# Performance work log

Hardware: AMD Instinct MI355X
Metric: run time of the kernel (lower is better)

The kernel has to match this reference:

```python
import jax, jax.numpy as jnp
import numpy as np

B, S, H = 2, 2048, 2048
NH = 16
HD = H // NH          # 128
ROT = HD // 4         # rotary_dim = head_dim * 0.25 = 32
VP = 320              # v_proj_dim
BASE = 10000.0


def setup_inputs() -> dict:
    key = jax.random.key(0)
    ks = jax.random.split(key, 10)
    sc = lambda fan_in: 1.0 / np.sqrt(fan_in)
    return {
        "hidden_states": jax.random.normal(ks[0], (B, S, H), jnp.float32),
        "Wqkv": jax.random.normal(ks[1], (3 * H, H), jnp.float32) * sc(H),
        "bqkv": jnp.zeros((3 * H,), jnp.float32),
        "Wc": jax.random.normal(ks[2], (VP, H), jnp.float32) * sc(H),
        "bc": jnp.zeros((VP,), jnp.float32),
        "Wr": jax.random.normal(ks[3], (H, VP), jnp.float32) * sc(VP),
        "br": jnp.zeros((H,), jnp.float32),
        "Wd": jax.random.normal(ks[4], (H, H), jnp.float32) * sc(H),
        "bd": jnp.zeros((H,), jnp.float32),
    }


def _rope_tables(seq_len, rot_dim, dtype):
    inv_freq = 1.0 / (BASE ** (jnp.arange(0, rot_dim, 2, dtype=jnp.float32) / rot_dim))
    t = jnp.arange(seq_len, dtype=jnp.float32)
    freqs = jnp.outer(t, inv_freq)                      # [S, rot/2]
    emb = jnp.concatenate([freqs, freqs], axis=-1)      # [S, rot]
    return jnp.cos(emb).astype(dtype), jnp.sin(emb).astype(dtype)


def _rotate_half(x):
    x1, x2 = jnp.split(x, 2, axis=-1)
    return jnp.concatenate([-x2, x1], axis=-1)


def reference(hidden_states, Wqkv, bqkv, Wc, bc, Wr, br, Wd, bd):
    b, s, h = hidden_states.shape
    qkv = hidden_states @ Wqkv.T + bqkv                 # [B,S,3H]
    qkv = qkv.reshape(b, s, 3, NH, HD)
    qkv = jnp.transpose(qkv, (2, 0, 3, 1, 4))           # [3,B,NH,S,HD]
    q, k, v = qkv[0], qkv[1], qkv[2]

    cos, sin = _rope_tables(s, ROT, hidden_states.dtype)  # [S,ROT]
    cos = cos[None, None, :, :]
    sin = sin[None, None, :, :]
    q_rot, q_pass = q[..., :ROT], q[..., ROT:]
    k_rot, k_pass = k[..., :ROT], k[..., ROT:]
    q_rot = q_rot * cos + _rotate_half(q_rot) * sin
    k_rot = k_rot * cos + _rotate_half(k_rot) * sin
    q = jnp.concatenate([q_rot, q_pass], axis=-1)
    k = jnp.concatenate([k_rot, k_pass], axis=-1)

    # V low-rank compress / restore
    v_hidden = jnp.transpose(v, (0, 2, 1, 3)).reshape(b, s, h)  # [B,S,H]
    v_restored = (v_hidden @ Wc.T + bc) @ Wr.T + br             # [B,S,H]
    v_heads = jnp.transpose(v_restored.reshape(b, s, NH, HD), (0, 2, 1, 3))  # [B,NH,S,HD]

    scale = HD ** -0.5
    scores = jnp.einsum('bhqd,bhkd->bhqk', q, k) * scale
    causal = jnp.triu(jnp.full((s, s), -jnp.inf, scores.dtype), k=1)
    scores = scores + causal
    attn = jax.nn.softmax(scores, axis=-1)
    out = jnp.einsum('bhqk,bhkd->bhqd', attn, v_heads)
    out = jnp.transpose(out, (0, 2, 1, 3)).reshape(b, s, h)
    return out @ Wd.T + bd
```

## Files before the change

kernel.cpp:

```cpp
#include <hip/hip_runtime.h>

typedef unsigned short u16;
typedef unsigned int u32;
typedef __bf16 bf16x8 __attribute__((ext_vector_type(8)));
typedef float f32x4 __attribute__((ext_vector_type(4)));

#define BB 2
#define SS 2048
#define HH 2048
#define NHH 16
#define HDD 128

__device__ __forceinline__ float b2f(u16 u) {
  union { u32 i; float f; } v; v.i = ((u32)u) << 16; return v.f;
}
__device__ __forceinline__ u16 f2b(float f) {
  union { float f; u32 i; } v; v.f = f;
  u32 x = v.i;
  u32 r = (x + 0x7fffu + ((x >> 16) & 1u)) >> 16;
  return (u16)r;
}

__device__ __forceinline__ void gload_lds16(const u16* g, u16* l) {
  __builtin_amdgcn_global_load_lds(
      (const __attribute__((address_space(1))) u32*)g,
      (__attribute__((address_space(3))) u32*)l, 16, 0, 0);
}

__global__ __launch_bounds__(256) void cvt_kernel(
    const float* __restrict__ s0, u16* __restrict__ d0, int n0,
    const float* __restrict__ s1, u16* __restrict__ d1, int n1,
    const float* __restrict__ s2, u16* __restrict__ d2, int n2,
    const float* __restrict__ s3, u16* __restrict__ d3, int n3,
    const float* __restrict__ s4, u16* __restrict__ d4, int n4)
{
  const float* s; u16* d; int n;
  switch (blockIdx.y) {
    case 0: s = s0; d = d0; n = n0; break;
    case 1: s = s1; d = d1; n = n1; break;
    case 2: s = s2; d = d2; n = n2; break;
    case 3: s = s3; d = d3; n = n3; break;
    default: s = s4; d = d4; n = n4; break;
  }
  int nq = n >> 2;
  for (int q = blockIdx.x * 256 + threadIdx.x; q < nq; q += gridDim.x * 256) {
    float4 v = *(const float4*)(s + (size_t)q * 4);
    ushort4 o;
    o.x = f2b(v.x); o.y = f2b(v.y); o.z = f2b(v.z); o.w = f2b(v.w);
    *(ushort4*)(d + (size_t)q * 4) = o;
  }
}

template<int OUT_F32, int ROPE, int BIAS_ROW>
__global__ __launch_bounds__(256) void gemm_bias_kernel(
    const u16* __restrict__ A, const u16* __restrict__ Bw,
    const float* __restrict__ bias, void* __restrict__ Cv,
    int M, int N, int K, int lda, int ldb, int ldc,
    size_t strideB, size_t strideC)
{
  __shared__ u16 Asf[128 * 4 * 8];
  __shared__ u16 Bsf[128 * 4 * 8];
  const int t = threadIdx.x;
  const int m0 = blockIdx.y * 128;
  const int n0 = blockIdx.x * 128;
  const int lane = t & 63, wid = t >> 6;
  const int wm = (wid >> 1) * 64, wn = (wid & 1) * 64;
  const int quad = lane >> 4, lm = lane & 15;

  const u16* Bz = Bw + (size_t)blockIdx.z * strideB;

  const int r16 = lane >> 2;
  const int swz = ((lane >> 2) & 3) ^ ((lane >> 4) & 3);
  const int kc = ((lane & 3) ^ swz) * 8;
  const int fswz = (lm & 3) ^ ((lm >> 2) & 3);

  f32x4 acc[4][4] = {};

  for (int k0 = 0; k0 < K; k0 += 32) {
    __syncthreads();
#pragma unroll
    for (int it = 0; it < 2; ++it) {
      int g = wid * 2 + it;
      int r = g * 16 + r16;
      gload_lds16(A + (size_t)(m0 + r) * lda + k0 + kc, &Asf[(size_t)g * 512]);
      gload_lds16(Bz + (size_t)(n0 + r) * ldb + k0 + kc, &Bsf[(size_t)g * 512]);
    }
    __syncthreads();
    bf16x8 af[4], bf[4];
#pragma unroll
    for (int i = 0; i < 4; ++i) {
      int row = wm + i * 16 + lm;
      af[i] = *(const bf16x8*)&Asf[(size_t)(row * 4 + (quad ^ fswz)) * 8];
    }
#pragma unroll
    for (int j = 0; j < 4; ++j) {
      int row = wn + j * 16 + lm;
      bf[j] = *(const bf16x8*)&Bsf[(size_t)(row * 4 + (quad ^ fswz)) * 8];
    }
#pragma unroll
    for (int i = 0; i < 4; ++i)
#pragma unroll
      for (int j = 0; j < 4; ++j)
        acc[i][j] = __builtin_amdgcn_mfma_f32_16x16x32_bf16(af[i], bf[j], acc[i][j], 0, 0, 0);
  }

  float* Cf = (float*)Cv + (OUT_F32 ? (size_t)blockIdx.z * strideC : 0);
  u16* Cu = (u16*)Cv + (OUT_F32 ? 0 : (size_t)blockIdx.z * strideC);
  const float ropefreq = ROPE ? exp2f(-(float)lm * 0.8304820237218406f) : 0.f;
  const bool do_rope = ROPE && (wn == 0) && (n0 < 4096);

#pragma unroll
  for (int i = 0; i < 4; ++i) {
    int gm = m0 + wm + i * 16 + quad * 4;
    int jstart = 0;
    if (do_rope) {
      jstart = 2;
      int gn0 = n0 + lm, gn1 = gn0 + 16;
      float b0 = bias[gn0], b1 = bias[gn1];
#pragma unroll
      for (int rg = 0; rg < 4; ++rg) {
        int rs = gm + rg;
        float sn, cs;
        sincosf((float)(rs & (SS - 1)) * ropefreq, &sn, &cs);
        float x0 = acc[i][0][rg] + b0, x1 = acc[i][1][rg] + b1;
        Cu[(size_t)rs * ldc + gn0] = f2b(x0 * cs - x1 * sn);
        Cu[(size_t)rs * ldc + gn1] = f2b(x1 * cs + x0 * sn);
      }
    }
#pragma unroll
    for (int j = 0; j < 4; ++j) {
      if (j < jstart) continue;
      int gn = n0 + wn + j * 16 + lm;
      if (gn < N) {
        f32x4 a = acc[i][j];
#pragma unroll
        for (int rg = 0; rg < 4; ++rg) {
          float bsv = BIAS_ROW ? bias[gm + rg] : bias[gn];
          if (OUT_F32) Cf[(size_t)(gm + rg) * ldc + gn] = a[rg] + bsv;
          else         Cu[(size_t)(gm + rg) * ldc + gn] = f2b(a[rg] + bsv);
        }
      }
    }
  }
}

__global__ __launch_bounds__(256) void attn_mfma_kernel(
    const u16* __restrict__ qkv, const u16* __restrict__ vrt, u16* __restrict__ out)
{
  __shared__ u16 Kt[64 * 16 * 8];
  __shared__ u16 Vt[8][128][8];
  __shared__ u16 Pa[4][16 * 64];

  const int t = threadIdx.x;
  const int lane = t & 63, w = t >> 6;
  const int quad = lane >> 4, lm = lane & 15;
  const int bx = blockIdx.x;
  const int bh = bx & 31;
  const int qt = 31 - (bx >> 5);
  const int b = bh >> 4, h = bh & 15;
  const int q0 = qt * 64;
  const int qw = q0 + w * 16;

  bf16x8 qf[4];
  {
    const u16* qsrc = qkv + (size_t)(b * SS + qw + lm) * 6144 + h * 128 + quad * 8;
#pragma unroll
    for (int dc = 0; dc < 4; ++dc) qf[dc] = *(const bf16x8*)(qsrc + dc * 32);
  }

  f32x4 Oa[8] = {};
  float m_i = -1e30f, l_i = 0.f;

  const float scale = 0.08838834764831845f;
  const int nkt = qt + 1;
  const u16* kbase = qkv + (size_t)b * SS * 6144 + 2048 + h * 128;
  const u16* vbase = vrt + (size_t)bh * 128 * 2048;
  u16* pw = &Pa[w][0];

  for (int kt = 0; kt < nkt; ++kt) {
    const int kb = kt * 64;
    __syncthreads();
#pragma unroll
    for (int it = 0; it < 4; ++it) {
      int c = t + it * 256;
      int kp = c >> 4, dq = c & 15;
      *(uint4*)&Kt[(size_t)(kp * 16 + (dq ^ (kp & 15))) * 8] =
          *(const uint4*)(kbase + (size_t)(kb + kp) * 6144 + dq * 8);
      int d = c >> 3, kq = c & 7;
      *(uint4*)&Vt[kq][d][0] =
          *(const uint4*)(vbase + (size_t)d * 2048 + kb + kq * 8);
    }
    __syncthreads();

    f32x4 sa[4] = {};
#pragma unroll
    for (int ct = 0; ct < 4; ++ct) {
#pragma unroll
      for (int dc = 0; dc < 4; ++dc) {
        bf16x8 kf = *(const bf16x8*)&Kt[(size_t)((ct * 16 + lm) * 16 +
                                                 ((dc * 4 + quad) ^ lm)) * 8];
        sa[ct] = __builtin_amdgcn_mfma_f32_16x16x32_bf16(kf, qf[dc], sa[ct], 0, 0, 0);
      }
    }
#pragma unroll
    for (int ct = 0; ct < 4; ++ct)
#pragma unroll
      for (int r = 0; r < 4; ++r) sa[ct][r] *= scale;

    if (kt == nkt - 1) {
      int qpos = qw + lm;
#pragma unroll
      for (int ct = 0; ct < 4; ++ct) {
#pragma unroll
        for (int r = 0; r < 4; ++r)
          if (kb + ct * 16 + quad * 4 + r > qpos) sa[ct][r] = -1e30f;
      }
    }

    float mx = sa[0][0];
#pragma unroll
    for (int ct = 0; ct < 4; ++ct)
#pragma unroll
      for (int r = 0; r < 4; ++r) mx = fmaxf(mx, sa[ct][r]);
    mx = fmaxf(mx, __shfl_xor(mx, 16, 64));
    mx = fmaxf(mx, __shfl_xor(mx, 32, 64));
    float mnew = fmaxf(m_i, mx);
    float alpha = __expf(m_i - mnew);
    float ssum = 0.f;
#pragma unroll
    for (int ct = 0; ct < 4; ++ct)
#pragma unroll
      for (int r = 0; r < 4; ++r) {
        float p = __expf(sa[ct][r] - mnew);
        sa[ct][r] = p;
        ssum += p;
      }
    ssum += __shfl_xor(ssum, 16, 64);
    ssum += __shfl_xor(ssum, 32, 64);
    l_i = l_i * alpha + ssum;
    m_i = mnew;

    float ar[4];
#pragma unroll
    for (int r = 0; r < 4; ++r) ar[r] = __shfl(alpha, quad * 4 + r, 64);
#pragma unroll
    for (int dt = 0; dt < 8; ++dt)
#pragma unroll
      for (int r = 0; r < 4; ++r) Oa[dt][r] *= ar[r];

#pragma unroll
    for (int ct = 0; ct < 4; ++ct) {
      uint2 pk;
      pk.x = (u32)f2b(sa[ct][0]) | ((u32)f2b(sa[ct][1]) << 16);
      pk.y = (u32)f2b(sa[ct][2]) | ((u32)f2b(sa[ct][3]) << 16);
      int u = ct * 2 + (quad >> 1);
      *(uint2*)(pw + lm * 64 + ((u ^ (lm & 7)) * 8) + (quad & 1) * 4) = pk;
    }
    bf16x8 pf0 = *(const bf16x8*)(pw + lm * 64 + ((quad ^ (lm & 7)) * 8));
    bf16x8 pf1 = *(const bf16x8*)(pw + lm * 64 + (((4 + quad) ^ (lm & 7)) * 8));

#pragma unroll
    for (int dt = 0; dt < 8; ++dt) {
      bf16x8 vf0 = *(const bf16x8*)&Vt[quad][dt * 16 + lm][0];
      bf16x8 vf1 = *(const bf16x8*)&Vt[4 + quad][dt * 16 + lm][0];
      Oa[dt] = __builtin_amdgcn_mfma_f32_16x16x32_bf16(pf0, vf0, Oa[dt], 0, 0, 0);
      Oa[dt] = __builtin_amdgcn_mfma_f32_16x16x32_bf16(pf1, vf1, Oa[dt], 0, 0, 0);
    }
  }

  float inv = 1.0f / l_i;
  float ir[4];
#pragma unroll
  for (int r = 0; r < 4; ++r) ir[r] = __shfl(inv, quad * 4 + r, 64);
  u16* dst = out + (size_t)(b * SS + qw + quad * 4) * 2048 + h * 128 + lm;
#pragma unroll
  for (int r = 0; r < 4; ++r)
#pragma unroll
    for (int dt = 0; dt < 8; ++dt)
      dst[(size_t)r * 2048 + dt * 16] = f2b(Oa[dt][r] * ir[r]);
}

extern "C" void kernel_launch(void* const* d_in, const int* in_sizes, int n_in,
                              void* d_out, int out_size, void* d_ws, size_t ws_size,
                              hipStream_t stream)
{
  (void)in_sizes; (void)n_in; (void)out_size; (void)ws_size;
  const float* X    = (const float*)d_in[0];
  const float* Wqkv = (const float*)d_in[1];
  const float* bqkv = (const float*)d_in[2];
  const float* Wc   = (const float*)d_in[3];
  const float* bc   = (const float*)d_in[4];
  const float* Wr   = (const float*)d_in[5];
  const float* br   = (const float*)d_in[6];
  const float* Wd   = (const float*)d_in[7];
  const float* bd   = (const float*)d_in[8];
  float* out = (float*)d_out;

  char* ws = (char*)d_ws;
  u16* QKV   = (u16*)(ws);
  u16* Xb    = (u16*)(ws + 50331648);
  u16* AO    = (u16*)(ws + 50331648);
  u16* Wqkvb = (u16*)(ws + 67108864);
  u16* VrT   = (u16*)(ws + 67108864);
  u16* Wcb   = (u16*)(ws + 92274688);
  u16* Wrb   = (u16*)(ws + 93585408);
  u16* Cb    = (u16*)(ws + 94896128);
  u16* Wdb   = (u16*)(ws + 97517568);

  dim3 blk(256);

  cvt_kernel<<<dim3(512, 5), blk, 0, stream>>>(
      X, Xb, 4096 * 2048,
      Wqkv, Wqkvb, 6144 * 2048,
      Wc, Wcb, 320 * 2048,
      Wr, Wrb, 2048 * 320,
      Wd, Wdb, 2048 * 2048);

  gemm_bias_kernel<0, 1, 0><<<dim3(48, 32), blk, 0, stream>>>(
      Xb, Wqkvb, bqkv, QKV, 4096, 6144, 2048, 2048, 2048, 6144, 0, 0);
  gemm_bias_kernel<0, 0, 0><<<dim3(3, 32), blk, 0, stream>>>(
      QKV + 4096, Wcb, bc, Cb, 4096, 320, 2048, 6144, 2048, 320, 0, 0);
  gemm_bias_kernel<0, 0, 1><<<dim3(16, 16, 2), blk, 0, stream>>>(
      Wrb, Cb, br, VrT, 2048, 2048, 320, 320, 320, 2048,
      (size_t)2048 * 320, (size_t)4194304);
  attn_mfma_kernel<<<dim3(1024), blk, 0, stream>>>(QKV, VrT, AO);
  gemm_bias_kernel<1, 0, 0><<<dim3(16, 32), blk, 0, stream>>>(
      AO, Wdb, bd, out, 4096, 2048, 2048, 2048, 2048, 2048, 0, 0);
}
```

Before: 507.3 us.

## Replace QKV projection GEMM with 256x256 tiled, 8-wave pipelined MFMA kernel with fused RoPE

Adds a new QKV projection kernel using 256x256 output tiles and 512 threads. It double-buffers LDS loads with direct global-to-LDS copies, interleaves quarter-tile MFMA phases with barriers, and raises wave priority around the MFMA blocks. The RoPE rotation and bias are applied in the epilogue. Larger tiles are meant to cut global traffic per FLOP and hide load latency better, at the cost of higher LDS and register use, fewer blocks (384), and per-element scattered bf16 stores.

```diff
diff --git a/kernel.cpp b/kernel.cpp
--- a/kernel.cpp
+++ b/kernel.cpp
@@ -48,6 +48,161 @@
     ushort4 o;
     o.x = f2b(v.x); o.y = f2b(v.y); o.z = f2b(v.z); o.w = f2b(v.w);
     *(ushort4*)(d + (size_t)q * 4) = o;
+  }
+}
+
+
+template<int ISA>
+__device__ __forceinline__ void stage_half(
+    const u16* __restrict__ src, u16* ldsmat, int h,
+    int tb, int kb, int ld, int wid, int lane)
+{
+#pragma unroll
+  for (int l = 0; l < 2; ++l) {
+    const int i = wid * 2 + l;
+    const int rp = i * 8 + (lane >> 3);
+    int r;
+    if (ISA) r = (rp & 63) + ((rp >> 6) << 7) + h * 64;
+    else     r = ((rp >> 5) << 6) + h * 32 + (rp & 31);
+    const int c = (lane & 7) ^ (lane >> 3);
+    gload_lds16(src + (size_t)(tb + r) * ld + kb + c * 8,
+                ldsmat + (size_t)(h * 128 + i * 8) * 64);
+  }
+}
+
+#define BAR()   __builtin_amdgcn_s_barrier()
+#define PRIO1() __builtin_amdgcn_s_setprio(1)
+#define PRIO0() __builtin_amdgcn_s_setprio(0)
+
+#define LDA_READ(BP, MH) do {                                                  \
+  const u16* _p = (BP);                                                        \
+  _Pragma("unroll") for (int mi = 0; mi < 4; ++mi) {                           \
+    const int _rho = (MH) * 128 + wr * 64 + mi * 16 + lm;                      \
+    _Pragma("unroll") for (int ks = 0; ks < 2; ++ks)                           \
+      af[mi][ks] = *(const bf16x8*)&_p[(size_t)_rho * 64 +                     \
+                                       ((((ks << 2) + quad) ^ (lm & 7)) << 3)];\
+  }                                                                            \
+} while (0)
+
+#define LDB_READ(BP, NH) do {                                                  \
+  const u16* _p = (BP);                                                        \
+  _Pragma("unroll") for (int ni = 0; ni < 2; ++ni) {                           \
+    const int _rho = (NH) * 128 + wc * 32 + ni * 16 + lm;                      \
+    _Pragma("unroll") for (int ks = 0; ks < 2; ++ks)                           \
+      bfr[NH][ni][ks] = *(const bf16x8*)&_p[(size_t)_rho * 64 +                \
+                                       ((((ks << 2) + quad) ^ (lm & 7)) << 3)];\
+  }                                                                            \
+} while (0)
+
+#define MFMA_Q(MH, NH) do {                                                    \
+  _Pragma("unroll") for (int mi = 0; mi < 4; ++mi)                             \
+    _Pragma("unroll") for (int ni = 0; ni < 2; ++ni)                           \
+      _Pragma("unroll") for (int ks = 0; ks < 2; ++ks)                         \
+        acc[(MH) * 4 + mi][(NH) * 2 + ni] =                                    \
+            __builtin_amdgcn_mfma_f32_16x16x32_bf16(                           \
+                af[mi][ks], bfr[NH][ni][ks],                                   \
+                acc[(MH) * 4 + mi][(NH) * 2 + ni], 0, 0, 0);                   \
+} while (0)
+
+__global__ __launch_bounds__(512, 2) void gemm256_rope_kernel(
+    const u16* __restrict__ A, const u16* __restrict__ Bw,
+    const float* __restrict__ bias, u16* __restrict__ C,
+    int M, int N, int K, int lda, int ldb, int ldc)
+{
+  __shared__ u16 lds[2][2][256 * 64];
+  const int t = threadIdx.x;
+  const int lane = t & 63, wid = t >> 6;
+  const int wr = wid >> 2, wc = wid & 3;
+  const int quad = lane >> 4, lm = lane & 15;
+  const int m0 = blockIdx.y * 256, n0 = blockIdx.x * 256;
+
+  u16* As0 = &lds[0][0][0]; u16* Bs0 = &lds[0][1][0];
+  u16* As1 = &lds[1][0][0]; u16* Bs1 = &lds[1][1][0];
+
+  f32x4 acc[8][4] = {};
+  bf16x8 af[4][2];
+  bf16x8 bfr[2][2][2];
+
+  const int NT = K >> 6;
+
+  stage_half<1>(A,  As0, 0, m0, 0, lda, wid, lane);
+  stage_half<0>(Bw, Bs0, 0, n0, 0, ldb, wid, lane);
+  stage_half<0>(Bw, Bs0, 1, n0, 0, ldb, wid, lane);
+  stage_half<1>(A,  As0, 1, m0, 0, lda, wid, lane);
+  asm volatile("s_waitcnt vmcnt(4)" ::: "memory");
+  stage_half<1>(A,  As1, 0, m0, 64, lda, wid, lane);
+  stage_half<0>(Bw, Bs1, 0, n0, 64, ldb, wid, lane);
+  stage_half<0>(Bw, Bs1, 1, n0, 64, ldb, wid, lane);
+  asm volatile("s_waitcnt vmcnt(6)" ::: "memory");
+  BAR();
+
+  for (int it2 = 0; it2 < (NT >> 1); ++it2) {
+    int kb1 = (it2 * 2 + 1) << 6;
+    int kb2 = (it2 * 2 + 2) << 6; if (kb2 >= K) kb2 -= K;
+    int kb3 = (it2 * 2 + 3) << 6; if (kb3 >= K) kb3 -= K;
+
+    LDA_READ(As0, 0); LDB_READ(Bs0, 0);
+    stage_half<1>(A, As1, 1, m0, kb1, lda, wid, lane);
+    BAR(); PRIO1(); MFMA_Q(0, 0); PRIO0(); BAR();
+    LDB_READ(Bs0, 1);
+    stage_half<1>(A, As0, 0, m0, kb2, lda, wid, lane);
+    BAR(); PRIO1(); MFMA_Q(0, 1); PRIO0(); BAR();
+    LDA_READ(As0, 1);
+    stage_half<0>(Bw, Bs0, 0, n0, kb2, ldb, wid, lane);
+    BAR(); PRIO1(); MFMA_Q(1, 1); PRIO0(); BAR();
+    stage_half<0>(Bw, Bs0, 1, n0, kb2, ldb, wid, lane);
+    asm volatile("s_waitcnt vmcnt(6)" ::: "memory");
+    BAR(); PRIO1(); MFMA_Q(1, 0); PRIO0(); BAR();
+    LDA_READ(As1, 0); LDB_READ(Bs1, 0);
+    stage_half<1>(A, As0, 1, m0, kb2, lda, wid, lane);
+    BAR(); PRIO1(); MFMA_Q(0, 0); PRIO0(); BAR();
+    LDB_READ(Bs1, 1);
+    stage_half<1>(A, As1, 0, m0, kb3, lda, wid, lane);
+    BAR(); PRIO1(); MFMA_Q(0, 1); PRIO0(); BAR();
+    LDA_READ(As1, 1);
+    stage_half<0>(Bw, Bs1, 0, n0, kb3, ldb, wid, lane);
+    BAR(); PRIO1(); MFMA_Q(1, 1); PRIO0(); BAR();
+    stage_half<0>(Bw, Bs1, 1, n0, kb3, ldb, wid, lane);
+    asm volatile("s_waitcnt vmcnt(6)" ::: "memory");
+    BAR(); PRIO1(); MFMA_Q(1, 0); PRIO0(); BAR();
+  }
+  asm volatile("s_waitcnt vmcnt(0)" ::: "memory");
+
+  const int cbase = n0 + wc * 64;
+  const float ropefreq = exp2f(-(float)lm * 0.8304820237218406f);
+  const bool do_rope = ((wc & 1) == 0) && (cbase < 4096);
+  float b0 = 0.f, b1 = 0.f;
+  if (do_rope) { b0 = bias[cbase + lm]; b1 = bias[cbase + lm + 16]; }
+
+#pragma unroll
+  for (int mi8 = 0; mi8 < 8; ++mi8) {
+    const int gm = m0 + wr * 128 + mi8 * 16 + quad * 4;
+    int jstart = 0;
+    if (do_rope) {
+      jstart = 2;
+      const int gn0 = cbase + lm, gn1 = gn0 + 16;
+#pragma unroll
+      for (int rg = 0; rg < 4; ++rg) {
+        int rs = gm + rg;
+        float sn, cs;
+        sincosf((float)(rs & (SS - 1)) * ropefreq, &sn, &cs);
+        float x0 = acc[mi8][0][rg] + b0, x1 = acc[mi8][1][rg] + b1;
+        C[(size_t)rs * ldc + gn0] = f2b(x0 * cs - x1 * sn);
+        C[(size_t)rs * ldc + gn1] = f2b(x1 * cs + x0 * sn);
+      }
+    }
+#pragma unroll
+    for (int nj = 0; nj < 4; ++nj) {
+      if (nj < jstart) continue;
+      const int gn = cbase + nj * 16 + lm;
+      if (gn < N) {
+        f32x4 a = acc[mi8][nj];
+        float bs = bias[gn];
+#pragma unroll
+        for (int rg = 0; rg < 4; ++rg)
+          C[(size_t)(gm + rg) * ldc + gn] = f2b(a[rg] + bs);
+      }
+    }
   }
 }
 
@@ -316,8 +471,8 @@
       Wr, Wrb, 2048 * 320,
       Wd, Wdb, 2048 * 2048);
 
-  gemm_bias_kernel<0, 1, 0><<<dim3(48, 32), blk, 0, stream>>>(
-      Xb, Wqkvb, bqkv, QKV, 4096, 6144, 2048, 2048, 2048, 6144, 0, 0);
+  gemm256_rope_kernel<<<dim3(24, 16), dim3(512), 0, stream>>>(
+      Xb, Wqkvb, bqkv, QKV, 4096, 6144, 2048, 2048, 2048, 6144);
   gemm_bias_kernel<0, 0, 0><<<dim3(3, 32), blk, 0, stream>>>(
       QKV + 4096, Wcb, bc, Cb, 4096, 320, 2048, 6144, 2048, 320, 0, 0);
   gemm_bias_kernel<0, 0, 1><<<dim3(16, 16, 2), blk, 0, stream>>>(
```

After: 493.6 us. 1.03x faster.
